# Performance work log

Measured on AMD Instinct MI355X. Metric: run time of the kernel, lower is better.

Reference implementation:

```python
import jax, jax.numpy as jnp
import numpy as np

B, N, C, K, H, W = 2, 16, 256, 64, 64, 64
NUM_HEADS = 8


def setup_inputs() -> dict:
    key = jax.random.key(0)
    ks = jax.random.split(key, 7)
    return {
        "value": jax.random.normal(ks[0], (B, N, C, H, W), dtype=jnp.float32),
        "key_map": jax.random.normal(ks[1], (B, K, H, W), dtype=jnp.float32),
        "state": jax.random.normal(ks[2], (B, N, K, C), dtype=jnp.float32),
        "b_w": jax.random.normal(ks[3], (NUM_HEADS, C), dtype=jnp.float32) * 0.06,
        "a_w": jax.random.normal(ks[4], (NUM_HEADS, C), dtype=jnp.float32) * 0.06,
        "A_log": jax.random.normal(ks[5], (NUM_HEADS,), dtype=jnp.float32),
        "dt_bias": jax.random.normal(ks[6], (NUM_HEADS,), dtype=jnp.float32),
    }


def reference(value, key_map, state, b_w, a_w, A_log, dt_bias):
    # Gated delta-rule erase-write memory update (state != None branch).
    num_heads = b_w.shape[0]
    rep = value.shape[2] // num_heads  # value_dim // num_heads

    # softmax over key channel dim (stable; matches max-subtract + softmax)
    key_n = jax.nn.softmax(key_map, axis=1)  # [B,K,H,W]

    # v_k = einsum('bkhw, bjhw,bnjv -> bnkv'): fuse via key gram matrix
    # (avoids materializing v_old [B,N,C,H,W])
    gram = jnp.einsum('bkhw,bjhw->bkj', key_n, key_n)      # [B,K,K]
    v_k = jnp.einsum('bkj,bnjv->bnkv', gram, state)        # [B,N,K,C]

    # erase gate beta: sigmoid(state @ b_proj^T), repeat over head groups
    beta = jax.nn.sigmoid(jnp.einsum('bnkc,hc->bnkh', state, b_w))
    beta = jnp.repeat(beta, rep, axis=3)                   # [B,N,K,C]

    # write term
    vk_t = jnp.einsum('bkhw,bnvhw->bnkv', key_n, value)    # [B,N,K,C]

    # decay gate alpha = -exp(A_log) * softplus(state @ a_proj^T + dt_bias)
    alpha = -jnp.exp(A_log) * jax.nn.softplus(
        jnp.einsum('bnkc,hc->bnkh', state, a_w) + dt_bias)
    alpha = jnp.repeat(alpha, rep, axis=3)                 # [B,N,K,C]

    new_state = alpha * (state - beta * v_k) + beta * vk_t  # [B,N,K,C]

    readout = jnp.einsum('bkhw,bnkv->bnvhw', key_n, new_state)  # [B,N,C,H,W]
    return readout
```

## Files before the change

### kernel.cpp

```cpp
#include <hip/hip_runtime.h>
#include <hip/hip_bf16.h>

#define BB 2
#define NN 16
#define CC 256
#define KK 64
#define HW 4096
#define NH 8

typedef __attribute__((ext_vector_type(4))) float f32x4;
typedef __attribute__((ext_vector_type(8))) short s16x8;
typedef __attribute__((ext_vector_type(4))) short s16x4;

__device__ __forceinline__ short f2bf(float f) {
    __hip_bfloat16 h = __float2bfloat16(f);
    return *reinterpret_cast<short*>(&h);
}
__device__ __forceinline__ float bf2f(short s) {
    unsigned int u = ((unsigned int)(unsigned short)s) << 16;
    float f; __builtin_memcpy(&f, &u, 4); return f;
}

__global__ __launch_bounds__(256) void k_pre(const float* __restrict__ state,
                                             const float* __restrict__ b_w,
                                             const float* __restrict__ a_w,
                                             const float* __restrict__ A_log,
                                             const float* __restrict__ dt_bias,
                                             float* __restrict__ betaH,
                                             float* __restrict__ alphaH,
                                             const float* __restrict__ km,
                                             short* __restrict__ kbf,
                                             short* __restrict__ kbfT) {
    __shared__ float red[4][2 * NH];
    const int tid = threadIdx.x;
    const int bid = blockIdx.x;

    if (bid < BB * NN * KK) {
        const int id = bid;
        const int bn = id >> 6;
        const int k = id & 63;
        const float s = state[((size_t)bn * KK + k) * CC + tid];

        float pb[NH], pa[NH];
#pragma unroll
        for (int h = 0; h < NH; h++) {
            pb[h] = s * b_w[h * CC + tid];
            pa[h] = s * a_w[h * CC + tid];
        }
#pragma unroll
        for (int off = 32; off; off >>= 1) {
#pragma unroll
            for (int h = 0; h < NH; h++) {
                pb[h] += __shfl_down(pb[h], off, 64);
                pa[h] += __shfl_down(pa[h], off, 64);
            }
        }
        const int wave = tid >> 6, lane = tid & 63;
        if (lane == 0) {
#pragma unroll
            for (int h = 0; h < NH; h++) { red[wave][h] = pb[h]; red[wave][NH + h] = pa[h]; }
        }
        __syncthreads();
        const int h = tid >> 5;
        float braw = 0.f, araw = 0.f;
#pragma unroll
        for (int w = 0; w < 4; w++) { braw += red[w][h]; araw += red[w][NH + h]; }
        if ((tid & 31) == 0) {
            const float beta = 1.f / (1.f + __expf(-braw));
            const float xx = araw + dt_bias[h];
            const float sp = fmaxf(xx, 0.f) + log1pf(__expf(-fabsf(xx)));
            const float alpha = -__expf(A_log[h]) * sp;
            betaH[(size_t)id * NH + h] = beta;
            alphaH[(size_t)id * NH + h] = alpha;
        }
    } else {
        const int sid = bid - BB * NN * KK;
        const int b = sid >> 5;
        const int w = tid >> 6, lane = tid & 63;
        const int hw = (sid & 31) * 128 + w * 32 + (lane & 31);
        const int half = lane >> 5;
        const float* p = km + ((size_t)b * KK + half * 32) * HW + hw;
        float x[32];
        float m = -1e30f;
#pragma unroll
        for (int k = 0; k < 32; k++) { x[k] = p[(size_t)k * HW]; m = fmaxf(m, x[k]); }
        m = fmaxf(m, __shfl_xor(m, 32, 64));
        float s = 0.f;
#pragma unroll
        for (int k = 0; k < 32; k++) { x[k] = __expf(x[k] - m); s += x[k]; }
        s += __shfl_xor(s, 32, 64);
        const float inv = 1.f / s;
        short* q2 = kbf + ((size_t)b * KK + half * 32) * HW + hw;
#pragma unroll
        for (int k = 0; k < 32; k++) {
            x[k] *= inv;
            q2[(size_t)k * HW] = f2bf(x[k]);
        }
        short* q3 = kbfT + ((size_t)b * HW + hw) * KK + half * 32;
#pragma unroll
        for (int k8 = 0; k8 < 32; k8 += 8) {
            s16x8 v;
#pragma unroll
            for (int j = 0; j < 8; j++) v[j] = f2bf(x[k8 + j]);
            *(s16x8*)(q3 + k8) = v;
        }
    }
}

__global__ __launch_bounds__(256) void k_gram(const short* __restrict__ kbf,
                                              float* __restrict__ gram) {
    const int tid = threadIdx.x;
    const int id = blockIdx.x;
    const int b = (id >= 2080) ? 1 : 0;
    const int t = id - b * 2080;
    int k = (int)((sqrtf(8.f * (float)t + 1.f) - 1.f) * 0.5f);
    while ((k + 1) * (k + 2) / 2 <= t) k++;
    while (k * (k + 1) / 2 > t) k--;
    const int j = t - k * (k + 1) / 2;

    const short* pa = kbf + ((size_t)b * KK + k) * HW + tid * 16;
    const short* pb = kbf + ((size_t)b * KK + j) * HW + tid * 16;
    const s16x8 a0 = *(const s16x8*)pa, a1 = *(const s16x8*)(pa + 8);
    const s16x8 b0 = *(const s16x8*)pb, b1 = *(const s16x8*)(pb + 8);
    float s = 0.f;
#pragma unroll
    for (int i = 0; i < 8; i++) {
        s = fmaf(bf2f(a0[i]), bf2f(b0[i]), s);
        s = fmaf(bf2f(a1[i]), bf2f(b1[i]), s);
    }
#pragma unroll
    for (int off = 32; off; off >>= 1) s += __shfl_down(s, off, 64);
    __shared__ float red[4];
    if ((tid & 63) == 0) red[tid >> 6] = s;
    __syncthreads();
    if (tid == 0) {
        const float tot = red[0] + red[1] + red[2] + red[3];
        gram[((size_t)b * KK + k) * KK + j] = tot;
        gram[((size_t)b * KK + j) * KK + k] = tot;
    }
}

__global__ __launch_bounds__(512) void k_vkt_part(const short* __restrict__ kbf,
                                                  const float* __restrict__ value,
                                                  float* __restrict__ pbuf) {
    const int tid = threadIdx.x;
    const int id = blockIdx.x;
    const int hs = id & 7;
    const int bn = id >> 3;
    const int b  = bn >> 4;
    const int w = tid >> 6, lane = tid & 63;
    const int l15 = lane & 15, hi = lane >> 4;
    const int hw0 = hs * 512;

    __shared__ short Bs[2][256 * 64];
    __shared__ short As[2][64 * 64];

    const int sr = tid >> 3;
    const int sj = tid & 7;
    const float* vbase = value + (size_t)bn * CC * HW + hw0;
    const short* abase = kbf + ((size_t)b * KK + sr) * HW + hw0 + sj * 8;

    f32x4 stgB[2][4][2];
    s16x8 stgA[2];

#define LOADREG(set_, t_)                                                      \
    {                                                                          \
        _Pragma("unroll") for (int i = 0; i < 4; i++) {                        \
            const float* p_ = vbase + (size_t)(sr + i * 64) * HW               \
                              + (t_) * 64 + sj * 8;                            \
            stgB[set_][i][0] = *(const f32x4*)p_;                              \
            stgB[set_][i][1] = *(const f32x4*)(p_ + 4);                        \
        }                                                                      \
        stgA[set_] = *(const s16x8*)(abase + (t_) * 64);                       \
    }
#define WRITE_LDS(set_, buf_)                                                  \
    {                                                                          \
        _Pragma("unroll") for (int i = 0; i < 4; i++) {                        \
            const int r_ = sr + i * 64;                                        \
            s16x8 tv_;                                                         \
            _Pragma("unroll") for (int e = 0; e < 4; e++) {                    \
                tv_[e]     = f2bf(stgB[set_][i][0][e]);                        \
                tv_[4 + e] = f2bf(stgB[set_][i][1][e]);                        \
            }                                                                  \
            *(s16x8*)&Bs[buf_][r_ * 64 + ((sj ^ (r_ & 7)) * 8)] = tv_;         \
        }                                                                      \
        *(s16x8*)&As[buf_][sr * 64 + ((sj ^ (sr & 7)) * 8)] = stgA[set_];      \
    }

    f32x4 acc[2][4];
#pragma unroll
    for (int m2 = 0; m2 < 2; m2++)
#pragma unroll
        for (int n4 = 0; n4 < 4; n4++) acc[m2][n4] = (f32x4){0.f, 0.f, 0.f, 0.f};

    LOADREG(0, 0);
    LOADREG(1, 1);
    WRITE_LDS(0, 0);
    asm volatile("s_waitcnt lgkmcnt(0)" ::: "memory");
    __builtin_amdgcn_s_barrier();

#pragma unroll
    for (int t = 0; t < 8; t++) {
        const int buf = t & 1;
        if (t + 2 < 8) LOADREG(buf, t + 2);

        const int swz = l15 & 7;
#pragma unroll
        for (int s = 0; s < 2; s++) {
            s16x8 vfr[2];
#pragma unroll
            for (int m2 = 0; m2 < 2; m2++)
                vfr[m2] = *(const s16x8*)&Bs[buf][(w * 32 + m2 * 16 + l15) * 64 +
                                                 (((s * 4 + hi) ^ swz) * 8)];
#pragma unroll
            for (int n4 = 0; n4 < 4; n4++) {
                const s16x8 afr = *(const s16x8*)&As[buf][(n4 * 16 + l15) * 64 +
                                                          (((s * 4 + hi) ^ swz) * 8)];
                acc[0][n4] = __builtin_amdgcn_mfma_f32_16x16x32_bf16(vfr[0], afr,
                                                                     acc[0][n4], 0, 0, 0);
                acc[1][n4] = __builtin_amdgcn_mfma_f32_16x16x32_bf16(vfr[1], afr,
                                                                     acc[1][n4], 0, 0, 0);
            }
        }
        asm volatile("s_waitcnt lgkmcnt(0)" ::: "memory");
        __builtin_amdgcn_s_barrier();
        if (t + 1 < 8) {
            WRITE_LDS((t + 1) & 1, (t + 1) & 1);
            asm volatile("s_waitcnt lgkmcnt(0)" ::: "memory");
            __builtin_amdgcn_s_barrier();
        }
    }
#undef LOADREG
#undef WRITE_LDS

    float* op = pbuf + (size_t)id * (KK * CC);
#pragma unroll
    for (int m2 = 0; m2 < 2; m2++)
#pragma unroll
        for (int n4 = 0; n4 < 4; n4++) {
            const int k = n4 * 16 + l15;
            const int c = w * 32 + m2 * 16 + hi * 4;
            *(f32x4*)(op + k * CC + c) = acc[m2][n4];
        }
}

__global__ __launch_bounds__(256) void k_combine(const float* __restrict__ pbuf,
                                                 const float* __restrict__ gram,
                                                 const float* __restrict__ state,
                                                 const float* __restrict__ betaH,
                                                 const float* __restrict__ alphaH,
                                                 short* __restrict__ nsT) {
    const int tid = threadIdx.x;
    const int id = blockIdx.x;
    const int ct = id & 15;
    const int bn = id >> 4;
    const int b  = bn >> 4;
    const int head = ct >> 1;

    __shared__ float gramL[KK][65];
    __shared__ float stL[KK][17];
    __shared__ float alphaL[KK], betaL[KK];
    __shared__ float nsb[KK][17];

    for (int i = tid; i < KK * KK; i += 256)
        gramL[i >> 6][i & 63] = gram[(size_t)b * KK * KK + i];
    for (int i = tid; i < KK * 16; i += 256)
        stL[i >> 4][i & 15] = state[((size_t)bn * KK + (i >> 4)) * CC + ct * 16 + (i & 15)];
    if (tid < KK) {
        alphaL[tid] = alphaH[((size_t)bn * KK + tid) * NH + head];
        betaL[tid]  = betaH[((size_t)bn * KK + tid) * NH + head];
    }
    __syncthreads();

    const int k = tid >> 2, cq = (tid & 3) * 4;

    f32x4 vkt = (f32x4){0.f, 0.f, 0.f, 0.f};
#pragma unroll
    for (int hs = 0; hs < 8; hs++) {
        const f32x4 p = *(const f32x4*)(pbuf + ((size_t)(bn * 8 + hs) * KK + k) * CC +
                                        ct * 16 + cq);
        vkt += p;
    }

    float vk[4] = {0.f, 0.f, 0.f, 0.f};
#pragma unroll 8
    for (int j = 0; j < KK; j++) {
        const float g = gramL[k][j];
        vk[0] = fmaf(g, stL[j][cq + 0], vk[0]);
        vk[1] = fmaf(g, stL[j][cq + 1], vk[1]);
        vk[2] = fmaf(g, stL[j][cq + 2], vk[2]);
        vk[3] = fmaf(g, stL[j][cq + 3], vk[3]);
    }
    const float al = alphaL[k], be = betaL[k];
#pragma unroll
    for (int i = 0; i < 4; i++)
        nsb[k][cq + i] = al * (stL[k][cq + i] - be * vk[i]) + be * vkt[i];
    __syncthreads();

    const int c = tid >> 4, k4 = (tid & 15) * 4;
    s16x4 v;
#pragma unroll
    for (int i = 0; i < 4; i++) v[i] = f2bf(nsb[k4 + i][c]);
    *(s16x4*)(nsT + ((size_t)bn * CC + ct * 16 + c) * KK + k4) = v;
}

__global__ __launch_bounds__(256) void k_readout_mfma(const short* __restrict__ kbfT,
                                                      const short* __restrict__ nsT,
                                                      float* __restrict__ out) {
    const int tid = threadIdx.x;
    const int id = blockIdx.x;
    const int hwt = id & 63;
    const int bn  = id >> 6;
    const int b   = bn >> 4;
    const int w = tid >> 6, lane = tid & 63;
    const int l15 = lane & 15, hi = lane >> 4;
    const int hw0 = hwt * 64 + w * 16;

    const short* Bp = kbfT + ((size_t)b * HW + hw0 + l15) * KK + hi * 8;
    const s16x8 hwf0 = *(const s16x8*)Bp;
    const s16x8 hwf1 = *(const s16x8*)(Bp + 32);

    const short* Ap = nsT + ((size_t)bn * CC + l15) * KK + hi * 8;
    float* op = out + ((size_t)bn * CC + l15) * HW + hw0 + hi * 4;

#pragma unroll
    for (int ct = 0; ct < 16; ct++) {
        const s16x8 a0 = *(const s16x8*)(Ap + (size_t)(ct * 16) * KK);
        const s16x8 a1 = *(const s16x8*)(Ap + (size_t)(ct * 16) * KK + 32);
        f32x4 acc = (f32x4){0.f, 0.f, 0.f, 0.f};
        acc = __builtin_amdgcn_mfma_f32_16x16x32_bf16(hwf0, a0, acc, 0, 0, 0);
        acc = __builtin_amdgcn_mfma_f32_16x16x32_bf16(hwf1, a1, acc, 0, 0, 0);
        *(f32x4*)(op + (size_t)(ct * 16) * HW) = acc;
    }
}

extern "C" void kernel_launch(void* const* d_in, const int* in_sizes, int n_in,
                              void* d_out, int out_size, void* d_ws, size_t ws_size,
                              hipStream_t stream) {
    const float* value   = (const float*)d_in[0];
    const float* key_map = (const float*)d_in[1];
    const float* state   = (const float*)d_in[2];
    const float* b_w     = (const float*)d_in[3];
    const float* a_w     = (const float*)d_in[4];
    const float* A_log   = (const float*)d_in[5];
    const float* dt_bias = (const float*)d_in[6];
    float* out = (float*)d_out;

    short* kbf   = (short*)d_ws;
    short* kbfT  = kbf + 524288;
    float* gram  = (float*)(kbfT + 524288);
    float* betaH = gram + 8192;
    float* alphaH= betaH + 16384;
    short* nsT   = (short*)(alphaH + 16384);
    float* pbuf  = (float*)(nsT + 524288);

    k_pre<<<BB * NN * KK + BB * (HW / 128), 256, 0, stream>>>(
        state, b_w, a_w, A_log, dt_bias, betaH, alphaH, key_map, kbf, kbfT);
    k_gram<<<BB * (KK * (KK + 1) / 2), 256, 0, stream>>>(kbf, gram);
    k_vkt_part<<<BB * NN * 8, 512, 0, stream>>>(kbf, value, pbuf);
    k_combine<<<BB * NN * 16, 256, 0, stream>>>(pbuf, gram, state, betaH, alphaH, nsT);
    k_readout_mfma<<<BB * NN * (HW / 64), 256, 0, stream>>>(kbfT, nsT, out);
}
```

Before: 104.9 us.

## Split vkt reduction into 16 HW slabs, store bf16 partials in fragment layout

The value·key write-term kernel now splits HW into 16 slabs of 256 instead of 8 of 512, doubling the grid to 512 blocks. The aim is better occupancy across the CUs on a kernel that is bound by reading value. Partial sums are written as bf16 in the MFMA fragment order, and the combine kernel reads and sums 16 such partials. The pipeline also moves the LDS write of the next tile ahead of the compute, dropping one barrier per iteration. Storing partials in bf16 adds rounding error to the summed write term, and the reduced barrier count could open an LDS race if the buffer indexing is wrong.

Result: faster. 101.4 us (-3.4%).

```diff
diff --git a/kernel.cpp b/kernel.cpp
--- a/kernel.cpp
+++ b/kernel.cpp
@@ -142,15 +142,15 @@
 
 __global__ __launch_bounds__(512) void k_vkt_part(const short* __restrict__ kbf,
                                                   const float* __restrict__ value,
-                                                  float* __restrict__ pbuf) {
+                                                  short* __restrict__ pbuf) {
     const int tid = threadIdx.x;
     const int id = blockIdx.x;
-    const int hs = id & 7;
-    const int bn = id >> 3;
+    const int hs = id & 15;
+    const int bn = id >> 4;
     const int b  = bn >> 4;
     const int w = tid >> 6, lane = tid & 63;
     const int l15 = lane & 15, hi = lane >> 4;
-    const int hw0 = hs * 512;
+    const int hw0 = hs * 256;
 
     __shared__ short Bs[2][256 * 64];
     __shared__ short As[2][64 * 64];
@@ -200,9 +200,10 @@
     __builtin_amdgcn_s_barrier();
 
 #pragma unroll
-    for (int t = 0; t < 8; t++) {
+    for (int t = 0; t < 4; t++) {
         const int buf = t & 1;
-        if (t + 2 < 8) LOADREG(buf, t + 2);
+        if (t + 2 < 4) LOADREG(buf, t + 2);
+        if (t + 1 < 4) WRITE_LDS((t + 1) & 1, (t + 1) & 1);
 
         const int swz = l15 & 7;
 #pragma unroll
@@ -222,10 +223,7 @@
                                                                      acc[1][n4], 0, 0, 0);
             }
         }
-        asm volatile("s_waitcnt lgkmcnt(0)" ::: "memory");
-        __builtin_amdgcn_s_barrier();
-        if (t + 1 < 8) {
-            WRITE_LDS((t + 1) & 1, (t + 1) & 1);
+        if (t + 1 < 4) {
             asm volatile("s_waitcnt lgkmcnt(0)" ::: "memory");
             __builtin_amdgcn_s_barrier();
         }
@@ -233,18 +231,19 @@
 #undef LOADREG
 #undef WRITE_LDS
 
-    float* op = pbuf + (size_t)id * (KK * CC);
 #pragma unroll
     for (int m2 = 0; m2 < 2; m2++)
 #pragma unroll
         for (int n4 = 0; n4 < 4; n4++) {
-            const int k = n4 * 16 + l15;
-            const int c = w * 32 + m2 * 16 + hi * 4;
-            *(f32x4*)(op + k * CC + c) = acc[m2][n4];
-        }
-}
-
-__global__ __launch_bounds__(256) void k_combine(const float* __restrict__ pbuf,
+            s16x4 v;
+#pragma unroll
+            for (int r = 0; r < 4; r++) v[r] = f2bf(acc[m2][n4][r]);
+            *(s16x4*)(pbuf + ((((size_t)(id * 8 + w) * 2 + m2) * 4 + n4) * 64
+                              + lane) * 4) = v;
+        }
+}
+
+__global__ __launch_bounds__(256) void k_combine(const short* __restrict__ pbuf,
                                                  const float* __restrict__ gram,
                                                  const float* __restrict__ state,
                                                  const float* __restrict__ betaH,
@@ -256,6 +255,7 @@
     const int bn = id >> 4;
     const int b  = bn >> 4;
     const int head = ct >> 1;
+    const int wi = ct >> 1, m2 = ct & 1;
 
     __shared__ float gramL[KK][65];
     __shared__ float stL[KK][17];
@@ -273,13 +273,16 @@
     __syncthreads();
 
     const int k = tid >> 2, cq = (tid & 3) * 4;
-
-    f32x4 vkt = (f32x4){0.f, 0.f, 0.f, 0.f};
-#pragma unroll
-    for (int hs = 0; hs < 8; hs++) {
-        const f32x4 p = *(const f32x4*)(pbuf + ((size_t)(bn * 8 + hs) * KK + k) * CC +
-                                        ct * 16 + cq);
-        vkt += p;
+    const int n4 = k >> 4, l15k = k & 15, hi = tid & 3;
+
+    float vkt[4] = {0.f, 0.f, 0.f, 0.f};
+#pragma unroll
+    for (int hs = 0; hs < 16; hs++) {
+        const int slab = bn * 16 + hs;
+        const s16x4 p = *(const s16x4*)(pbuf +
+            ((((size_t)(slab * 8 + wi) * 2 + m2) * 4 + n4) * 64 + hi * 16 + l15k) * 4);
+#pragma unroll
+        for (int i = 0; i < 4; i++) vkt[i] += bf2f(p[i]);
     }
 
     float vk[4] = {0.f, 0.f, 0.f, 0.f};
@@ -352,12 +355,12 @@
     float* betaH = gram + 8192;
     float* alphaH= betaH + 16384;
     short* nsT   = (short*)(alphaH + 16384);
-    float* pbuf  = (float*)(nsT + 524288);
+    short* pbufB = nsT + 524288;
 
     k_pre<<<BB * NN * KK + BB * (HW / 128), 256, 0, stream>>>(
         state, b_w, a_w, A_log, dt_bias, betaH, alphaH, key_map, kbf, kbfT);
     k_gram<<<BB * (KK * (KK + 1) / 2), 256, 0, stream>>>(kbf, gram);
-    k_vkt_part<<<BB * NN * 8, 512, 0, stream>>>(kbf, value, pbuf);
-    k_combine<<<BB * NN * 16, 256, 0, stream>>>(pbuf, gram, state, betaH, alphaH, nsT);
+    k_vkt_part<<<BB * NN * 16, 512, 0, stream>>>(kbf, value, pbufB);
+    k_combine<<<BB * NN * 16, 256, 0, stream>>>(pbufB, gram, state, betaH, alphaH, nsT);
     k_readout_mfma<<<BB * NN * (HW / 64), 256, 0, stream>>>(kbfT, nsT, out);
 }
```
